# Performance work log

Hardware: AMD Instinct MI355X
Metric: run time of the kernel (lower is better)

## Reference

```python
import jax, jax.numpy as jnp
import numpy as np

N_HEADS = 4
N_HIDDEN = 64  # out_features // n_heads
NEG_SLOPE = 0.2


def setup_inputs() -> dict:
    key = jax.random.key(0)
    k1, k2, k3, k4, k5 = jax.random.split(key, 5)
    B, N, F_IN, F_OUT = 1, 4096, 128, 256
    h = jax.random.normal(k1, (B, N, F_IN), dtype=jnp.float32)
    adj_mat = jax.random.uniform(k2, (N, N, 1), dtype=jnp.float32)
    W_proj = jax.random.normal(k3, (F_IN, N_HEADS * N_HIDDEN), dtype=jnp.float32) / np.sqrt(F_IN)
    W_proj_attn = jax.random.normal(k4, (F_IN, N_HEADS * N_HIDDEN // 2), dtype=jnp.float32) / np.sqrt(F_IN)
    w_attn = jax.random.normal(k5, (N_HIDDEN,), dtype=jnp.float32) / np.sqrt(N_HIDDEN)
    return {"h": h, "adj_mat": adj_mat, "W_proj": W_proj, "W_proj_attn": W_proj_attn, "w_attn": w_attn}


def reference(h, adj_mat, W_proj, W_proj_attn, w_attn):
    B, N, _ = h.shape
    H, D = N_HEADS, N_HIDDEN
    half = D // 2
    # value projection: (B, N, H, D)
    g = (h @ W_proj).reshape(B, N, H, D)
    # attention-feature projection: (B, N, H, D//2)
    ga = (h @ W_proj_attn).reshape(B, N, H, half)
    # attn(cat([ga_i, ga_j])) decomposes linearly: e_ij = <w_l, ga_i> + <w_r, ga_j>
    # (identical math to the torch repeat/cat/Linear, without the NxNxD tensor)
    el = jnp.einsum('bnhk,k->bnh', ga, w_attn[:half])   # dest node i term
    er = jnp.einsum('bnhk,k->bnh', ga, w_attn[half:])   # source node j term
    e = jax.nn.leaky_relu(el[:, :, None, :] + er[:, None, :, :], NEG_SLOPE)  # (B, N, N, H)
    mask = adj_mat >= 0.5  # (N, N, 1) broadcasts over (B, N, N, H)
    e = jnp.where(mask, e, -jnp.inf)
    a = jax.nn.softmax(e, axis=2)  # softmax over source nodes j
    # dropout is identity in eval mode
    out = jnp.einsum('bijh,bjhf->bihf', a, g)  # (B, N, H, D)
    return out.reshape(B, N, H * D)  # is_concat=True
```

## Files before the change

### kernel.cpp

```cpp
#include <hip/hip_runtime.h>
#include <hip/hip_bf16.h>

typedef __bf16 bf16_t;
typedef __bf16 bf16x4 __attribute__((ext_vector_type(4)));
typedef __bf16 bf16x8 __attribute__((ext_vector_type(8)));
typedef float floatx4 __attribute__((ext_vector_type(4)));

#define N_NODES 4096
#define F_IN 128
#define NUM_HEADS 4
#define D_HID 64
#define F_OUT 256
#define NEG_SLOPE 0.2f

__device__ __forceinline__ void async_copy16(const void* gsrc, void* ldst)
{
    __builtin_amdgcn_global_load_lds(
        (const __attribute__((address_space(1))) unsigned int*)gsrc,
        (__attribute__((address_space(3))) unsigned int*)ldst,
        16, 0, 0);
}

__global__ __launch_bounds__(384) void proj_kernel(
    const float* __restrict__ hmat, const float* __restrict__ Wp,
    const float* __restrict__ Wa, const float* __restrict__ wattn,
    bf16_t* __restrict__ GB, float* __restrict__ el, float* __restrict__ er)
{
    const int t = threadIdx.x;
    const int j0 = blockIdx.x * 4;

    float acc[4] = {0.f, 0.f, 0.f, 0.f};

    const float* wptr;
    int stride;
    if (t < 256) { wptr = Wp + t;         stride = 256; }
    else         { wptr = Wa + (t - 256); stride = 128; }

    const float* hbase = hmat + (size_t)j0 * F_IN;

    for (int m = 0; m < F_IN; m += 4) {
        const float w0 = wptr[(size_t)(m + 0) * stride];
        const float w1 = wptr[(size_t)(m + 1) * stride];
        const float w2 = wptr[(size_t)(m + 2) * stride];
        const float w3 = wptr[(size_t)(m + 3) * stride];
#pragma unroll
        for (int jl = 0; jl < 4; ++jl) {
            const float4 hv = *reinterpret_cast<const float4*>(&hbase[jl * F_IN + m]);
            acc[jl] = fmaf(hv.w, w3, fmaf(hv.z, w2, fmaf(hv.y, w1, fmaf(hv.x, w0, acc[jl]))));
        }
    }

    if (t < 256) {
        const int h = t >> 6, f = t & 63;
        bf16x4 o;
#pragma unroll
        for (int q = 0; q < 4; ++q) o[q] = (bf16_t)acc[q];
        const size_t base = ((((size_t)h * 128 + (j0 >> 5)) * 4 + (f >> 4)) * 64
                             + (f & 15) + 16 * ((j0 >> 3) & 3)) * 8 + (j0 & 7);
        *reinterpret_cast<bf16x4*>(&GB[base]) = o;
    } else {
        const int ta = t - 256;
        const int ha = ta >> 5, k = ta & 31;
        const float wl = wattn[k], wr = wattn[32 + k];
#pragma unroll
        for (int jl = 0; jl < 4; ++jl) {
            float vl = acc[jl] * wl;
            float vr = acc[jl] * wr;
#pragma unroll
            for (int s = 16; s >= 1; s >>= 1) {
                vl += __shfl_xor(vl, s, 64);
                vr += __shfl_xor(vr, s, 64);
            }
            if (k == 0) {
                el[ha * N_NODES + j0 + jl] = vl;
                er[ha * N_NODES + j0 + jl] = vr;
            }
        }
    }
}

__global__ __launch_bounds__(512, 6) void attn_kernel(
    const float* __restrict__ adj, const bf16_t* __restrict__ GB,
    const float* __restrict__ el, const float* __restrict__ er,
    float* __restrict__ numout, float* __restrict__ den_g,
    int njc, int ntiles)
{
    __shared__ bf16_t P_s[NUM_HEADS * 32 * 64];
    __shared__ bf16_t GB_s[32 * 512];

    const int tid = threadIdx.x;
    const int i0  = blockIdx.x * 32;
    const int jc  = blockIdx.y;
    const int jT0 = jc * ntiles * 64;

    const int pi   = tid >> 4;
    const int pj4  = (tid & 15) << 2;
    const int glog = pj4 >> 3;
    const int goff = pj4 & 7;
    const int psw  = ((glog ^ (pi & 7)) << 3) + goff;

    const int wave = tid >> 6;
    const int hh   = wave >> 1;
    const int mt   = wave & 1;
    const int lane = tid & 63;
    const int m    = lane & 15;
    const int quad = lane >> 4;

    float elr[NUM_HEADS];
#pragma unroll
    for (int h = 0; h < NUM_HEADS; ++h) elr[h] = el[h * N_NODES + i0 + pi];

    const float* adjp = adj + (size_t)(i0 + pi) * N_NODES + pj4;

    const int sb = wave * 4;

    floatx4 acc0 = {0.f, 0.f, 0.f, 0.f};
    floatx4 acc1 = acc0, acc2 = acc0, acc3 = acc0, accd = acc0;
    bf16x8 ones;
#pragma unroll
    for (int q = 0; q < 8; ++q) ones[q] = (bf16_t)1.0f;

    float4 adjv = *reinterpret_cast<const float4*>(adjp + jT0);

    for (int k = 0; k < ntiles; ++k) {
        const int jT   = jT0 + k * 64;
        const int jb32 = jT >> 5;
#pragma unroll
        for (int q = 0; q < 4; ++q) {
            const int s  = sb + q;
            const int sj = s >> 4, sh = (s >> 2) & 3, sf = s & 3;
            const bf16_t* gsrc =
                GB + ((size_t)(sh * 128 + jb32 + sj) * 4 + sf) * 512 + lane * 8;
            async_copy16(gsrc, &GB_s[s * 512 + lane * 8]);
        }
        float4 adjn;
        if (k + 1 < ntiles)
            adjn = *reinterpret_cast<const float4*>(adjp + jT + 64);
        const bool k0 = adjv.x >= 0.5f, k1 = adjv.y >= 0.5f,
                   k2 = adjv.z >= 0.5f, k3 = adjv.w >= 0.5f;
#pragma unroll
        for (int h = 0; h < NUM_HEADS; ++h) {
            const float4 ev = *reinterpret_cast<const float4*>(er + h * N_NODES + jT + pj4);
            float e0 = elr[h] + ev.x, e1 = elr[h] + ev.y,
                  e2 = elr[h] + ev.z, e3 = elr[h] + ev.w;
            e0 = fmaxf(e0, NEG_SLOPE * e0);
            e1 = fmaxf(e1, NEG_SLOPE * e1);
            e2 = fmaxf(e2, NEG_SLOPE * e2);
            e3 = fmaxf(e3, NEG_SLOPE * e3);
            bf16x4 pv;
            pv[0] = (bf16_t)(k0 ? __expf(e0) : 0.f);
            pv[1] = (bf16_t)(k1 ? __expf(e1) : 0.f);
            pv[2] = (bf16_t)(k2 ? __expf(e2) : 0.f);
            pv[3] = (bf16_t)(k3 ? __expf(e3) : 0.f);
            *reinterpret_cast<bf16x4*>(&P_s[(h * 32 + pi) * 64 + psw]) = pv;
        }
        __syncthreads();
        __builtin_amdgcn_s_setprio(1);
#pragma unroll
        for (int kt = 0; kt < 2; ++kt) {
            const int gphys = (((kt * 4 + quad) ^ (m & 7)) << 3);
            const bf16x8 af = *reinterpret_cast<const bf16x8*>(
                &P_s[(hh * 32 + mt * 16 + m) * 64 + gphys]);
            accd = __builtin_amdgcn_mfma_f32_16x16x32_bf16(af, ones, accd, 0, 0, 0);
            const int bb = (kt * 16 + hh * 4) * 512 + lane * 8;
            const bf16x8 b0 = *reinterpret_cast<const bf16x8*>(&GB_s[bb]);
            const bf16x8 b1 = *reinterpret_cast<const bf16x8*>(&GB_s[bb + 512]);
            const bf16x8 b2 = *reinterpret_cast<const bf16x8*>(&GB_s[bb + 1024]);
            const bf16x8 b3 = *reinterpret_cast<const bf16x8*>(&GB_s[bb + 1536]);
            acc0 = __builtin_amdgcn_mfma_f32_16x16x32_bf16(af, b0, acc0, 0, 0, 0);
            acc1 = __builtin_amdgcn_mfma_f32_16x16x32_bf16(af, b1, acc1, 0, 0, 0);
            acc2 = __builtin_amdgcn_mfma_f32_16x16x32_bf16(af, b2, acc2, 0, 0, 0);
            acc3 = __builtin_amdgcn_mfma_f32_16x16x32_bf16(af, b3, acc3, 0, 0, 0);
        }
        __builtin_amdgcn_s_setprio(0);
        if (k + 1 < ntiles) adjv = adjn;
        __syncthreads();
    }

    const int ibase = i0 + mt * 16 + quad * 4;
    if (njc == 1) {
#pragma unroll
        for (int r = 0; r < 4; ++r) {
            const float rd = 1.0f / accd[r];
            float* dst = numout + (size_t)(ibase + r) * F_OUT + hh * D_HID + m;
            dst[0]  = acc0[r] * rd;
            dst[16] = acc1[r] * rd;
            dst[32] = acc2[r] * rd;
            dst[48] = acc3[r] * rd;
        }
    } else {
        float* nrow = numout + (size_t)jc * ((size_t)N_NODES * F_OUT);
#pragma unroll
        for (int r = 0; r < 4; ++r) {
            float* dst = nrow + (size_t)(ibase + r) * F_OUT + hh * D_HID + m;
            dst[0]  = acc0[r];
            dst[16] = acc1[r];
            dst[32] = acc2[r];
            dst[48] = acc3[r];
        }
        if (m == 0) {
#pragma unroll
            for (int r = 0; r < 4; ++r)
                den_g[((size_t)jc * N_NODES + ibase + r) * NUM_HEADS + hh] = accd[r];
        }
    }
}

template<int NJC>
__global__ __launch_bounds__(256) void reduce_kernel(
    const float* __restrict__ num, const float* __restrict__ den,
    float* __restrict__ out)
{
    const int idx = blockIdx.x * 256 + threadIdx.x;
    const int i  = idx >> 8;
    const int c  = idx & 255;
    const int hh = c >> 6;
    float n = 0.f, d = 0.f;
#pragma unroll
    for (int jc = 0; jc < NJC; ++jc) {
        n += num[(size_t)jc * ((size_t)N_NODES * F_OUT) + idx];
        d += den[((size_t)jc * N_NODES + i) * NUM_HEADS + hh];
    }
    out[idx] = n / d;
}

extern "C" void kernel_launch(void* const* d_in, const int* in_sizes, int n_in,
                              void* d_out, int out_size, void* d_ws, size_t ws_size,
                              hipStream_t stream)
{
    const float* hmat = (const float*)d_in[0];
    const float* adj  = (const float*)d_in[1];
    const float* Wp   = (const float*)d_in[2];
    const float* Wa   = (const float*)d_in[3];
    const float* watt = (const float*)d_in[4];
    float* out = (float*)d_out;

    char* ws = (char*)d_ws;
    bf16_t* GB = (bf16_t*)ws;
    float*  el = (float*)(ws + (2ull << 20));
    float*  er = (float*)(ws + (2ull << 20) + (64ull << 10));
    const size_t baseoff = (2ull << 20) + (128ull << 10);

    const size_t num_bytes = (size_t)N_NODES * F_OUT * 4;
    const size_t den_bytes = (size_t)N_NODES * NUM_HEADS * 4;
    const int njc = (ws_size >= baseoff + 8 * (num_bytes + den_bytes)) ? 8
                  : (ws_size >= baseoff + 4 * (num_bytes + den_bytes)) ? 4 : 2;

    float* num = (float*)(ws + baseoff);
    float* den = (float*)(ws + baseoff + (size_t)njc * num_bytes);

    proj_kernel<<<1024, 384, 0, stream>>>(hmat, Wp, Wa, watt, GB, el, er);
    attn_kernel<<<dim3(128, njc), 512, 0, stream>>>(adj, GB, el, er, num, den,
                                                    njc, (N_NODES / njc) / 64);
    if (njc == 8)      reduce_kernel<8><<<(N_NODES * F_OUT) / 256, 256, 0, stream>>>(num, den, out);
    else if (njc == 4) reduce_kernel<4><<<(N_NODES * F_OUT) / 256, 256, 0, stream>>>(num, den, out);
    else               reduce_kernel<2><<<(N_NODES * F_OUT) / 256, 256, 0, stream>>>(num, den, out);
}
```

Before: 153.5 us.

## Compute attention probabilities directly in MFMA A-fragment registers, removing LDS staging

Restructures the attention kernel so each wave owns one head and two 16-row groups. Each lane computes its masked exp values straight into the bf16 MFMA A-operand layout and loads GB B-fragments directly from global memory, which removes the P and GB shared-memory buffers and both barriers per tile. The log2(e) factor is folded into el/er in the projection kernel so the exponent can use the hardware exp2. In exchange, adjacency and er are read redundantly across waves and GB is fetched without LDS reuse, and the njc==1 normalization path is dropped.

Measured after the change: 165.8 us. 8.0% more time.

```diff
diff --git a/kernel.cpp b/kernel.cpp
--- a/kernel.cpp
+++ b/kernel.cpp
@@ -12,14 +12,7 @@
 #define D_HID 64
 #define F_OUT 256
 #define NEG_SLOPE 0.2f
-
-__device__ __forceinline__ void async_copy16(const void* gsrc, void* ldst)
-{
-    __builtin_amdgcn_global_load_lds(
-        (const __attribute__((address_space(1))) unsigned int*)gsrc,
-        (__attribute__((address_space(3))) unsigned int*)ldst,
-        16, 0, 0);
-}
+#define LOG2E 1.4426950408889634f
 
 __global__ __launch_bounds__(384) void proj_kernel(
     const float* __restrict__ hmat, const float* __restrict__ Wp,
@@ -61,7 +54,7 @@
     } else {
         const int ta = t - 256;
         const int ha = ta >> 5, k = ta & 31;
-        const float wl = wattn[k], wr = wattn[32 + k];
+        const float wl = wattn[k] * LOG2E, wr = wattn[32 + k] * LOG2E;
 #pragma unroll
         for (int jl = 0; jl < 4; ++jl) {
             float vl = acc[jl] * wl;
@@ -79,129 +72,101 @@
     }
 }
 
-__global__ __launch_bounds__(512, 6) void attn_kernel(
+__global__ __launch_bounds__(256, 4) void attn_kernel(
     const float* __restrict__ adj, const bf16_t* __restrict__ GB,
     const float* __restrict__ el, const float* __restrict__ er,
     float* __restrict__ numout, float* __restrict__ den_g,
     int njc, int ntiles)
 {
-    __shared__ bf16_t P_s[NUM_HEADS * 32 * 64];
-    __shared__ bf16_t GB_s[32 * 512];
-
-    const int tid = threadIdx.x;
-    const int i0  = blockIdx.x * 32;
-    const int jc  = blockIdx.y;
-    const int jT0 = jc * ntiles * 64;
-
-    const int pi   = tid >> 4;
-    const int pj4  = (tid & 15) << 2;
-    const int glog = pj4 >> 3;
-    const int goff = pj4 & 7;
-    const int psw  = ((glog ^ (pi & 7)) << 3) + goff;
-
-    const int wave = tid >> 6;
-    const int hh   = wave >> 1;
-    const int mt   = wave & 1;
+    const int tid  = threadIdx.x;
+    const int i0   = blockIdx.x * 32;
+    const int jc   = blockIdx.y;
+    const int jT0  = jc * ntiles * 64;
+    const int hh   = tid >> 6;
     const int lane = tid & 63;
     const int m    = lane & 15;
     const int quad = lane >> 4;
 
-    float elr[NUM_HEADS];
-#pragma unroll
-    for (int h = 0; h < NUM_HEADS; ++h) elr[h] = el[h * N_NODES + i0 + pi];
-
-    const float* adjp = adj + (size_t)(i0 + pi) * N_NODES + pj4;
-
-    const int sb = wave * 4;
-
-    floatx4 acc0 = {0.f, 0.f, 0.f, 0.f};
-    floatx4 acc1 = acc0, acc2 = acc0, acc3 = acc0, accd = acc0;
+    const float el_lo = el[hh * N_NODES + i0 + m];
+    const float el_hi = el[hh * N_NODES + i0 + 16 + m];
+    const float* adj_lo = adj + (size_t)(i0 + m) * N_NODES;
+    const float* adj_hi = adj_lo + (size_t)16 * N_NODES;
+    const float* erp    = er + hh * N_NODES;
+    const bf16_t* gb_h  = GB + (size_t)hh * (128 * 4 * 512) + lane * 8;
+
+    floatx4 accL0 = {0.f, 0.f, 0.f, 0.f};
+    floatx4 accL1 = accL0, accL2 = accL0, accL3 = accL0, accdL = accL0;
+    floatx4 accH0 = accL0, accH1 = accL0, accH2 = accL0, accH3 = accL0, accdH = accL0;
     bf16x8 ones;
 #pragma unroll
     for (int q = 0; q < 8; ++q) ones[q] = (bf16_t)1.0f;
 
-    float4 adjv = *reinterpret_cast<const float4*>(adjp + jT0);
-
     for (int k = 0; k < ntiles; ++k) {
-        const int jT   = jT0 + k * 64;
-        const int jb32 = jT >> 5;
-#pragma unroll
-        for (int q = 0; q < 4; ++q) {
-            const int s  = sb + q;
-            const int sj = s >> 4, sh = (s >> 2) & 3, sf = s & 3;
-            const bf16_t* gsrc =
-                GB + ((size_t)(sh * 128 + jb32 + sj) * 4 + sf) * 512 + lane * 8;
-            async_copy16(gsrc, &GB_s[s * 512 + lane * 8]);
-        }
-        float4 adjn;
-        if (k + 1 < ntiles)
-            adjn = *reinterpret_cast<const float4*>(adjp + jT + 64);
-        const bool k0 = adjv.x >= 0.5f, k1 = adjv.y >= 0.5f,
-                   k2 = adjv.z >= 0.5f, k3 = adjv.w >= 0.5f;
-#pragma unroll
-        for (int h = 0; h < NUM_HEADS; ++h) {
-            const float4 ev = *reinterpret_cast<const float4*>(er + h * N_NODES + jT + pj4);
-            float e0 = elr[h] + ev.x, e1 = elr[h] + ev.y,
-                  e2 = elr[h] + ev.z, e3 = elr[h] + ev.w;
-            e0 = fmaxf(e0, NEG_SLOPE * e0);
-            e1 = fmaxf(e1, NEG_SLOPE * e1);
-            e2 = fmaxf(e2, NEG_SLOPE * e2);
-            e3 = fmaxf(e3, NEG_SLOPE * e3);
-            bf16x4 pv;
-            pv[0] = (bf16_t)(k0 ? __expf(e0) : 0.f);
-            pv[1] = (bf16_t)(k1 ? __expf(e1) : 0.f);
-            pv[2] = (bf16_t)(k2 ? __expf(e2) : 0.f);
-            pv[3] = (bf16_t)(k3 ? __expf(e3) : 0.f);
-            *reinterpret_cast<bf16x4*>(&P_s[(h * 32 + pi) * 64 + psw]) = pv;
-        }
-        __syncthreads();
-        __builtin_amdgcn_s_setprio(1);
+        const int jT = jT0 + k * 64;
 #pragma unroll
         for (int kt = 0; kt < 2; ++kt) {
-            const int gphys = (((kt * 4 + quad) ^ (m & 7)) << 3);
-            const bf16x8 af = *reinterpret_cast<const bf16x8*>(
-                &P_s[(hh * 32 + mt * 16 + m) * 64 + gphys]);
-            accd = __builtin_amdgcn_mfma_f32_16x16x32_bf16(af, ones, accd, 0, 0, 0);
-            const int bb = (kt * 16 + hh * 4) * 512 + lane * 8;
-            const bf16x8 b0 = *reinterpret_cast<const bf16x8*>(&GB_s[bb]);
-            const bf16x8 b1 = *reinterpret_cast<const bf16x8*>(&GB_s[bb + 512]);
-            const bf16x8 b2 = *reinterpret_cast<const bf16x8*>(&GB_s[bb + 1024]);
-            const bf16x8 b3 = *reinterpret_cast<const bf16x8*>(&GB_s[bb + 1536]);
-            acc0 = __builtin_amdgcn_mfma_f32_16x16x32_bf16(af, b0, acc0, 0, 0, 0);
-            acc1 = __builtin_amdgcn_mfma_f32_16x16x32_bf16(af, b1, acc1, 0, 0, 0);
-            acc2 = __builtin_amdgcn_mfma_f32_16x16x32_bf16(af, b2, acc2, 0, 0, 0);
-            acc3 = __builtin_amdgcn_mfma_f32_16x16x32_bf16(af, b3, acc3, 0, 0, 0);
-        }
-        __builtin_amdgcn_s_setprio(0);
-        if (k + 1 < ntiles) adjv = adjn;
-        __syncthreads();
-    }
-
-    const int ibase = i0 + mt * 16 + quad * 4;
-    if (njc == 1) {
+            const int jb = jT + kt * 32 + quad * 8;
+            const float4 aL0 = *reinterpret_cast<const float4*>(adj_lo + jb);
+            const float4 aL1 = *reinterpret_cast<const float4*>(adj_lo + jb + 4);
+            const float4 aH0 = *reinterpret_cast<const float4*>(adj_hi + jb);
+            const float4 aH1 = *reinterpret_cast<const float4*>(adj_hi + jb + 4);
+            const float4 e0  = *reinterpret_cast<const float4*>(erp + jb);
+            const float4 e1  = *reinterpret_cast<const float4*>(erp + jb + 4);
+            const bf16_t* gp = gb_h + (size_t)((jT >> 5) + kt) * (4 * 512);
+            const bf16x8 b0 = *reinterpret_cast<const bf16x8*>(gp);
+            const bf16x8 b1 = *reinterpret_cast<const bf16x8*>(gp + 512);
+            const bf16x8 b2 = *reinterpret_cast<const bf16x8*>(gp + 1024);
+            const bf16x8 b3 = *reinterpret_cast<const bf16x8*>(gp + 1536);
+
+            const float ev[8]  = {e0.x, e0.y, e0.z, e0.w, e1.x, e1.y, e1.z, e1.w};
+            const float avL[8] = {aL0.x, aL0.y, aL0.z, aL0.w, aL1.x, aL1.y, aL1.z, aL1.w};
+            const float avH[8] = {aH0.x, aH0.y, aH0.z, aH0.w, aH1.x, aH1.y, aH1.z, aH1.w};
+
+            bf16x8 afL, afH;
+#pragma unroll
+            for (int q = 0; q < 8; ++q) {
+                const float sL = el_lo + ev[q];
+                const float sH = el_hi + ev[q];
+                const float pL = __builtin_amdgcn_exp2f(fmaxf(sL, NEG_SLOPE * sL));
+                const float pH = __builtin_amdgcn_exp2f(fmaxf(sH, NEG_SLOPE * sH));
+                afL[q] = (bf16_t)(avL[q] >= 0.5f ? pL : 0.0f);
+                afH[q] = (bf16_t)(avH[q] >= 0.5f ? pH : 0.0f);
+            }
+
+            accdL = __builtin_amdgcn_mfma_f32_16x16x32_bf16(afL, ones, accdL, 0, 0, 0);
+            accdH = __builtin_amdgcn_mfma_f32_16x16x32_bf16(afH, ones, accdH, 0, 0, 0);
+            accL0 = __builtin_amdgcn_mfma_f32_16x16x32_bf16(afL, b0, accL0, 0, 0, 0);
+            accH0 = __builtin_amdgcn_mfma_f32_16x16x32_bf16(afH, b0, accH0, 0, 0, 0);
+            accL1 = __builtin_amdgcn_mfma_f32_16x16x32_bf16(afL, b1, accL1, 0, 0, 0);
+            accH1 = __builtin_amdgcn_mfma_f32_16x16x32_bf16(afH, b1, accH1, 0, 0, 0);
+            accL2 = __builtin_amdgcn_mfma_f32_16x16x32_bf16(afL, b2, accL2, 0, 0, 0);
+            accH2 = __builtin_amdgcn_mfma_f32_16x16x32_bf16(afH, b2, accH2, 0, 0, 0);
+            accL3 = __builtin_amdgcn_mfma_f32_16x16x32_bf16(afL, b3, accL3, 0, 0, 0);
+            accH3 = __builtin_amdgcn_mfma_f32_16x16x32_bf16(afH, b3, accH3, 0, 0, 0);
+        }
+    }
+
+    float* nrow = numout + (size_t)jc * ((size_t)N_NODES * F_OUT);
+    const int ibL = i0 + quad * 4;
+    const int ibH = ibL + 16;
+#pragma unroll
+    for (int r = 0; r < 4; ++r) {
+        float* dL = nrow + (size_t)(ibL + r) * F_OUT + hh * D_HID + m;
+        dL[0]  = accL0[r];
+        dL[16] = accL1[r];
+        dL[32] = accL2[r];
+        dL[48] = accL3[r];
+        float* dH = nrow + (size_t)(ibH + r) * F_OUT + hh * D_HID + m;
+        dH[0]  = accH0[r];
+        dH[16] = accH1[r];
+        dH[32] = accH2[r];
+        dH[48] = accH3[r];
+    }
+    if (m == 0) {
 #pragma unroll
         for (int r = 0; r < 4; ++r) {
-            const float rd = 1.0f / accd[r];
-            float* dst = numout + (size_t)(ibase + r) * F_OUT + hh * D_HID + m;
-            dst[0]  = acc0[r] * rd;
-            dst[16] = acc1[r] * rd;
-            dst[32] = acc2[r] * rd;
-            dst[48] = acc3[r] * rd;
-        }
-    } else {
-        float* nrow = numout + (size_t)jc * ((size_t)N_NODES * F_OUT);
-#pragma unroll
-        for (int r = 0; r < 4; ++r) {
-            float* dst = nrow + (size_t)(ibase + r) * F_OUT + hh * D_HID + m;
-            dst[0]  = acc0[r];
-            dst[16] = acc1[r];
-            dst[32] = acc2[r];
-            dst[48] = acc3[r];
-        }
-        if (m == 0) {
-#pragma unroll
-            for (int r = 0; r < 4; ++r)
-                den_g[((size_t)jc * N_NODES + ibase + r) * NUM_HEADS + hh] = accd[r];
+            den_g[((size_t)jc * N_NODES + ibL + r) * NUM_HEADS + hh] = accdL[r];
+            den_g[((size_t)jc * N_NODES + ibH + r) * NUM_HEADS + hh] = accdH[r];
         }
     }
 }
@@ -250,7 +215,7 @@
     float* den = (float*)(ws + baseoff + (size_t)njc * num_bytes);
 
     proj_kernel<<<1024, 384, 0, stream>>>(hmat, Wp, Wa, watt, GB, el, er);
-    attn_kernel<<<dim3(128, njc), 512, 0, stream>>>(adj, GB, el, er, num, den,
+    attn_kernel<<<dim3(128, njc), 256, 0, stream>>>(adj, GB, el, er, num, den,
                                                     njc, (N_NODES / njc) / 64);
     if (njc == 8)      reduce_kernel<8><<<(N_NODES * F_OUT) / 256, 256, 0, stream>>>(num, den, out);
     else if (njc == 4) reduce_kernel<4><<<(N_NODES * F_OUT) / 256, 256, 0, stream>>>(num, den, out);
```
